# Optimization experiments

Measured on AMD Instinct MI355X. Metric: run time of the kernel, lower is better.

Reference implementation:

```python
import jax, jax.numpy as jnp
import numpy as np

EPS = 1e-7

def sphere_log(p, q):
    # Riemannian log on unit sphere; p, q broadcastable, points along last axis.
    dot = jnp.clip(jnp.sum(p * q, axis=-1, keepdims=True), -1.0 + EPS, 1.0 - EPS)
    theta = jnp.arccos(dot)
    v = q - dot * p                      # tangent direction (unnormalized)
    nv = jnp.linalg.norm(v, axis=-1, keepdims=True)
    nv_safe = jnp.where(nv < EPS, 1.0, nv)
    factor = jnp.where(nv < EPS, 1.0, theta / nv_safe)  # theta/||v|| -> 1 as q->p
    return factor * v

def sphere_exp(p, v):
    # Riemannian exp on unit sphere.
    n = jnp.linalg.norm(v, axis=-1, keepdims=True)
    n_safe = jnp.where(n < EPS, 1.0, n)
    s = jnp.where(n < EPS, 1.0, jnp.sin(n_safe) / n_safe)  # sinc(||v||)
    return jnp.cos(n) * p + s * v

def setup_inputs() -> dict:
    key = jax.random.key(0)
    k1, k2 = jax.random.split(key)
    B, L, C_in, C_out, d = 4, 256, 64, 64, 64
    x = jax.random.normal(k1, (B, L, C_in, d), dtype=jnp.float32)
    x = x / jnp.linalg.norm(x, axis=-1, keepdims=True)  # points on S^{d-1}
    # param 'w': truncated_normal(stddev=1) with shape (n_in, n_out)
    w_raw = jax.random.truncated_normal(k2, -2.0, 2.0, (C_in, C_out), dtype=jnp.float32)
    return {"x": x, "w_raw": w_raw}

def reference(x, w_raw):
    B, L, C_in, d = x.shape
    C_out = w_raw.shape[1]
    # softmax-like positive, column-normalized weights
    w = jnp.exp(w_raw - np.log(C_in).astype(np.float32))
    w = w / w.sum(axis=0)[None]          # (C_in, C_out)

    xr = x.reshape(B * L, C_in, d)       # (N, C_in, d)
    # init at first in-channel point, broadcast over out channels: (N, C_out, d)
    a = jnp.broadcast_to(xr[:, 0][:, None, :], (B * L, C_out, d))

    # 3-step fixed-point iteration toward weighted Frechet mean (scan unroll=3)
    for _ in range(3):
        logs = sphere_log(a[:, :, None, :], xr[:, None, :, :])  # (N, C_out, C_in, d)
        grad = jnp.einsum('io,noid->nod', w, logs)              # (N, C_out, d)
        a = sphere_exp(a, grad)

    return a.reshape(B, L, C_out, d)
```

## Files before the change

kernel.cpp:

```cpp
#include <hip/hip_runtime.h>

#define EPSF 1e-7f
#define TS2 72
#define OFS 68

typedef __bf16 bf16;
typedef __attribute__((ext_vector_type(8))) __bf16 bf16x8;
typedef __attribute__((ext_vector_type(4))) __bf16 bf16x4;
typedef __attribute__((ext_vector_type(4))) float f32x4;

__device__ __forceinline__ float dpp_sum16(float v) {
  int x;
  x = __builtin_amdgcn_update_dpp(0, __builtin_bit_cast(int, v), 0xB1, 0xf, 0xf, true);
  v += __builtin_bit_cast(float, x);
  x = __builtin_amdgcn_update_dpp(0, __builtin_bit_cast(int, v), 0x4E, 0xf, 0xf, true);
  v += __builtin_bit_cast(float, x);
  x = __builtin_amdgcn_update_dpp(0, __builtin_bit_cast(int, v), 0x141, 0xf, 0xf, true);
  v += __builtin_bit_cast(float, x);
  x = __builtin_amdgcn_update_dpp(0, __builtin_bit_cast(int, v), 0x140, 0xf, 0xf, true);
  v += __builtin_bit_cast(float, x);
  return v;
}

__device__ __forceinline__ float fused_factor(float dot) {
  float ax = fabsf(dot);
  float q2 = __builtin_amdgcn_rsqf(1.0f + ax);
  float r2 = __builtin_amdgcn_rsqf(1.0f - ax);
  float pa = fmaf(fmaf(fmaf(-0.0187292994f, ax, 0.0742610070f), ax,
                       -0.2121144013f), ax, 1.5707288f);
  float sel = (dot < 0.0f) ? fmaf(3.14159265358979f, r2, -pa) : pa;
  return sel * q2;
}

__global__ __launch_bounds__(256, 4) void mfd_fc_mfma(
    const float* __restrict__ x, const float* __restrict__ wraw,
    float* __restrict__ out) {
  __shared__ __align__(16) char smem[3 * 64 * TS2 * sizeof(bf16)];
  bf16* Xrow = (bf16*)smem;
  bf16* Xt   = Xrow + 64 * TS2;
  bf16* AC   = Xt + 64 * TS2;
  float* OutF = (float*)smem;

  const int n = blockIdx.x;
  const int tid = threadIdx.x;
  const int wv = tid >> 6;
  const int lane = tid & 63;
  const int ln15 = lane & 15;
  const int quad = lane >> 4;
  const int obase = 16 * wv + 4 * quad;
  const float* xn = x + (size_t)n * 4096;

#pragma unroll
  for (int t = 0; t < 4; ++t) {
    int idx = tid + t * 256;
    int i = idx >> 4;
    int c4 = (idx & 15) << 2;
    float4 v = reinterpret_cast<const float4*>(xn)[idx];
    bf16x4 b;
    b[0] = (bf16)v.x; b[1] = (bf16)v.y; b[2] = (bf16)v.z; b[3] = (bf16)v.w;
    *reinterpret_cast<bf16x4*>(&Xrow[i * TS2 + c4]) = b;
  }

  float wf[4][4];
  {
    float cs[4] = {0.f, 0.f, 0.f, 0.f};
#pragma unroll
    for (int t = 0; t < 4; ++t) {
      float4 wr = *reinterpret_cast<const float4*>(&wraw[(16 * t + ln15) * 64 + obase]);
      wf[t][0] = __expf(wr.x); wf[t][1] = __expf(wr.y);
      wf[t][2] = __expf(wr.z); wf[t][3] = __expf(wr.w);
#pragma unroll
      for (int r = 0; r < 4; ++r) cs[r] += wf[t][r];
    }
#pragma unroll
    for (int r = 0; r < 4; ++r) {
      float inv = __builtin_amdgcn_rcpf(dpp_sum16(cs[r]));
#pragma unroll
      for (int t = 0; t < 4; ++t) wf[t][r] *= inv;
    }
  }

  float a_reg[4][4];
#pragma unroll
  for (int t = 0; t < 4; ++t) {
    float v = xn[16 * t + ln15];
#pragma unroll
    for (int r = 0; r < 4; ++r) a_reg[t][r] = v;
  }
#pragma unroll
  for (int t = 0; t < 4; ++t)
#pragma unroll
    for (int r = 0; r < 4; ++r)
      AC[(obase + r) * TS2 + 16 * t + ln15] = (bf16)a_reg[t][r];

  __syncthreads();

  {
    int dd = tid & 63, ih = tid >> 6;
    bf16 tmp[16];
#pragma unroll
    for (int j = 0; j < 16; ++j) tmp[j] = Xrow[(16 * ih + j) * TS2 + dd];
    *reinterpret_cast<bf16x8*>(&Xt[dd * TS2 + 16 * ih]) =
        *reinterpret_cast<bf16x8*>(&tmp[0]);
    *reinterpret_cast<bf16x8*>(&Xt[dd * TS2 + 16 * ih + 8]) =
        *reinterpret_cast<bf16x8*>(&tmp[8]);
  }

  bf16x8 xrf[4][2];
#pragma unroll
  for (int t = 0; t < 4; ++t)
#pragma unroll
    for (int ks = 0; ks < 2; ++ks)
      xrf[t][ks] = *reinterpret_cast<const bf16x8*>(
          &Xrow[(16 * t + ln15) * TS2 + ks * 32 + quad * 8]);

  const bf16* acbase = &AC[(16 * wv + ln15) * TS2];

  for (int it = 0; it < 3; ++it) {
    f32x4 acc[4] = {f32x4{0,0,0,0}, f32x4{0,0,0,0}, f32x4{0,0,0,0}, f32x4{0,0,0,0}};
#pragma unroll
    for (int ks = 0; ks < 2; ++ks) {
      bf16x8 af = *reinterpret_cast<const bf16x8*>(&acbase[ks * 32 + quad * 8]);
#pragma unroll
      for (int t = 0; t < 4; ++t)
        acc[t] = __builtin_amdgcn_mfma_f32_16x16x32_bf16(af, xrf[t][ks], acc[t], 0, 0, 0);
    }

    float sd[4] = {0.f, 0.f, 0.f, 0.f};
#pragma unroll
    for (int t = 0; t < 4; ++t) {
#pragma unroll
      for (int r = 0; r < 4; ++r) {
        float raw = acc[t][r];
        float dot = __builtin_amdgcn_fmed3f(raw, -1.0f + EPSF, 1.0f - EPSF);
        bf16 cb = (bf16)(wf[t][r] * fused_factor(dot));
        AC[(obase + r) * TS2 + 16 * t + ln15] = cb;
        sd[r] = fmaf((float)cb, dot, sd[r]);
      }
    }
#pragma unroll
    for (int r = 0; r < 4; ++r) sd[r] = dpp_sum16(sd[r]);

    if (it == 0) __syncthreads();

    f32x4 g[4] = {f32x4{0,0,0,0}, f32x4{0,0,0,0}, f32x4{0,0,0,0}, f32x4{0,0,0,0}};
#pragma unroll
    for (int ks = 0; ks < 2; ++ks) {
      bf16x8 af = *reinterpret_cast<const bf16x8*>(&acbase[ks * 32 + quad * 8]);
#pragma unroll
      for (int t = 0; t < 4; ++t) {
        bf16x8 bfr = *reinterpret_cast<const bf16x8*>(
            &Xt[(16 * t + ln15) * TS2 + ks * 32 + quad * 8]);
        g[t] = __builtin_amdgcn_mfma_f32_16x16x32_bf16(af, bfr, g[t], 0, 0, 0);
      }
    }

    float gn2[4] = {0.f, 0.f, 0.f, 0.f};
#pragma unroll
    for (int t = 0; t < 4; ++t)
#pragma unroll
      for (int r = 0; r < 4; ++r) {
        float v = g[t][r] - sd[r] * a_reg[t][r];
        g[t][r] = v;
        gn2[r] = fmaf(v, v, gn2[r]);
      }
#pragma unroll
    for (int r = 0; r < 4; ++r) {
      float nrm = __builtin_amdgcn_sqrtf(dpp_sum16(gn2[r]));
      float rev = nrm * 0.15915494309189535f;
      float sn_ = __builtin_amdgcn_sinf(rev);
      float cn  = __builtin_amdgcn_cosf(rev);
      float sn = (nrm < EPSF) ? 1.0f : sn_ * __builtin_amdgcn_rcpf(nrm);
#pragma unroll
      for (int t = 0; t < 4; ++t)
        a_reg[t][r] = fmaf(cn, a_reg[t][r], sn * g[t][r]);
    }
    if (it < 2) {
#pragma unroll
      for (int t = 0; t < 4; ++t)
#pragma unroll
        for (int r = 0; r < 4; ++r)
          AC[(obase + r) * TS2 + 16 * t + ln15] = (bf16)a_reg[t][r];
    }
  }

  __syncthreads();
#pragma unroll
  for (int t = 0; t < 4; ++t)
#pragma unroll
    for (int r = 0; r < 4; ++r)
      OutF[(obase + r) * OFS + 16 * t + ln15] = a_reg[t][r];
  __syncthreads();
  float* outn = out + (size_t)n * 4096;
#pragma unroll
  for (int t = 0; t < 4; ++t) {
    int idx = tid + t * 256;
    int row = idx >> 4, col4 = (idx & 15) << 2;
    float4 v = *reinterpret_cast<const float4*>(&OutF[row * OFS + col4]);
    reinterpret_cast<float4*>(outn)[idx] = v;
  }
}

extern "C" void kernel_launch(void* const* d_in, const int* in_sizes, int n_in,
                              void* d_out, int out_size, void* d_ws, size_t ws_size,
                              hipStream_t stream) {
  const float* x = (const float*)d_in[0];
  const float* wraw = (const float*)d_in[1];
  float* out = (float*)d_out;
  (void)d_ws; (void)ws_size;

  int N = in_sizes[0] / 4096;
  mfd_fc_mfma<<<N, 256, 0, stream>>>(x, wraw, out);
}
```

Measured before the change: 82.78 us.

## Skip first-iteration MFMA using shared init point and write output directly

At the first iteration every output channel starts from the same point x[0], so the dot products depend only on the input channel. The change computes them with a per-lane bf16 dot and shuffles instead of MFMA plus an AC staging write, and evaluates the arccos factor once per input channel. It also drops the LDS staging of the final output and its two barriers, writing results straight to global memory with 64-byte segments per row rather than float4-coalesced stores. The exchange is less efficient global store patterns for fewer barriers and LDS traffic.

After: 80.59 us. -2.6%, faster.

```diff
diff --git a/kernel.cpp b/kernel.cpp
--- a/kernel.cpp
+++ b/kernel.cpp
@@ -2,7 +2,6 @@
 
 #define EPSF 1e-7f
 #define TS2 72
-#define OFS 68
 
 typedef __bf16 bf16;
 typedef __attribute__((ext_vector_type(8))) __bf16 bf16x8;
@@ -39,7 +38,6 @@
   bf16* Xrow = (bf16*)smem;
   bf16* Xt   = Xrow + 64 * TS2;
   bf16* AC   = Xt + 64 * TS2;
-  float* OutF = (float*)smem;
 
   const int n = blockIdx.x;
   const int tid = threadIdx.x;
@@ -87,13 +85,21 @@
 #pragma unroll
     for (int r = 0; r < 4; ++r) a_reg[t][r] = v;
   }
+
+  __syncthreads();
+
+  bf16x8 xrf[4][2];
 #pragma unroll
   for (int t = 0; t < 4; ++t)
 #pragma unroll
-    for (int r = 0; r < 4; ++r)
-      AC[(obase + r) * TS2 + 16 * t + ln15] = (bf16)a_reg[t][r];
-
-  __syncthreads();
+    for (int ks = 0; ks < 2; ++ks)
+      xrf[t][ks] = *reinterpret_cast<const bf16x8*>(
+          &Xrow[(16 * t + ln15) * TS2 + ks * 32 + quad * 8]);
+
+  bf16x8 x0f[2];
+#pragma unroll
+  for (int ks = 0; ks < 2; ++ks)
+    x0f[ks] = *reinterpret_cast<const bf16x8*>(&Xrow[ks * 32 + quad * 8]);
 
   {
     int dd = tid & 63, ih = tid >> 6;
@@ -106,36 +112,49 @@
         *reinterpret_cast<bf16x8*>(&tmp[8]);
   }
 
-  bf16x8 xrf[4][2];
-#pragma unroll
-  for (int t = 0; t < 4; ++t)
-#pragma unroll
-    for (int ks = 0; ks < 2; ++ks)
-      xrf[t][ks] = *reinterpret_cast<const bf16x8*>(
-          &Xrow[(16 * t + ln15) * TS2 + ks * 32 + quad * 8]);
-
   const bf16* acbase = &AC[(16 * wv + ln15) * TS2];
 
   for (int it = 0; it < 3; ++it) {
-    f32x4 acc[4] = {f32x4{0,0,0,0}, f32x4{0,0,0,0}, f32x4{0,0,0,0}, f32x4{0,0,0,0}};
-#pragma unroll
-    for (int ks = 0; ks < 2; ++ks) {
-      bf16x8 af = *reinterpret_cast<const bf16x8*>(&acbase[ks * 32 + quad * 8]);
-#pragma unroll
-      for (int t = 0; t < 4; ++t)
-        acc[t] = __builtin_amdgcn_mfma_f32_16x16x32_bf16(af, xrf[t][ks], acc[t], 0, 0, 0);
-    }
-
     float sd[4] = {0.f, 0.f, 0.f, 0.f};
-#pragma unroll
-    for (int t = 0; t < 4; ++t) {
-#pragma unroll
-      for (int r = 0; r < 4; ++r) {
-        float raw = acc[t][r];
-        float dot = __builtin_amdgcn_fmed3f(raw, -1.0f + EPSF, 1.0f - EPSF);
-        bf16 cb = (bf16)(wf[t][r] * fused_factor(dot));
-        AC[(obase + r) * TS2 + 16 * t + ln15] = cb;
-        sd[r] = fmaf((float)cb, dot, sd[r]);
+    if (it == 0) {
+#pragma unroll
+      for (int t = 0; t < 4; ++t) {
+        float p = 0.f;
+#pragma unroll
+        for (int ks = 0; ks < 2; ++ks)
+#pragma unroll
+          for (int j = 0; j < 8; ++j)
+            p = fmaf((float)xrf[t][ks][j], (float)x0f[ks][j], p);
+        p += __shfl_xor(p, 16, 64);
+        p += __shfl_xor(p, 32, 64);
+        float d0 = __builtin_amdgcn_fmed3f(p, -1.0f + EPSF, 1.0f - EPSF);
+        float f0 = fused_factor(d0);
+#pragma unroll
+        for (int r = 0; r < 4; ++r) {
+          bf16 cb = (bf16)(wf[t][r] * f0);
+          AC[(obase + r) * TS2 + 16 * t + ln15] = cb;
+          sd[r] = fmaf((float)cb, d0, sd[r]);
+        }
+      }
+    } else {
+      f32x4 acc[4] = {f32x4{0,0,0,0}, f32x4{0,0,0,0}, f32x4{0,0,0,0}, f32x4{0,0,0,0}};
+#pragma unroll
+      for (int ks = 0; ks < 2; ++ks) {
+        bf16x8 af = *reinterpret_cast<const bf16x8*>(&acbase[ks * 32 + quad * 8]);
+#pragma unroll
+        for (int t = 0; t < 4; ++t)
+          acc[t] = __builtin_amdgcn_mfma_f32_16x16x32_bf16(af, xrf[t][ks], acc[t], 0, 0, 0);
+      }
+#pragma unroll
+      for (int t = 0; t < 4; ++t) {
+#pragma unroll
+        for (int r = 0; r < 4; ++r) {
+          float raw = acc[t][r];
+          float dot = __builtin_amdgcn_fmed3f(raw, -1.0f + EPSF, 1.0f - EPSF);
+          bf16 cb = (bf16)(wf[t][r] * fused_factor(dot));
+          AC[(obase + r) * TS2 + 16 * t + ln15] = cb;
+          sd[r] = fmaf((float)cb, dot, sd[r]);
+        }
       }
     }
 #pragma unroll
@@ -174,31 +193,20 @@
 #pragma unroll
       for (int t = 0; t < 4; ++t)
         a_reg[t][r] = fmaf(cn, a_reg[t][r], sn * g[t][r]);
-    }
-    if (it < 2) {
-#pragma unroll
-      for (int t = 0; t < 4; ++t)
-#pragma unroll
-        for (int r = 0; r < 4; ++r)
+      if (it < 2) {
+#pragma unroll
+        for (int t = 0; t < 4; ++t)
           AC[(obase + r) * TS2 + 16 * t + ln15] = (bf16)a_reg[t][r];
-    }
-  }
-
-  __syncthreads();
+      }
+    }
+  }
+
+  float* outn = out + (size_t)n * 4096;
 #pragma unroll
   for (int t = 0; t < 4; ++t)
 #pragma unroll
     for (int r = 0; r < 4; ++r)
-      OutF[(obase + r) * OFS + 16 * t + ln15] = a_reg[t][r];
-  __syncthreads();
-  float* outn = out + (size_t)n * 4096;
-#pragma unroll
-  for (int t = 0; t < 4; ++t) {
-    int idx = tid + t * 256;
-    int row = idx >> 4, col4 = (idx & 15) << 2;
-    float4 v = *reinterpret_cast<const float4*>(&OutF[row * OFS + col4]);
-    reinterpret_cast<float4*>(outn)[idx] = v;
-  }
+      outn[(obase + r) * 64 + 16 * t + ln15] = a_reg[t][r];
 }
 
 extern "C" void kernel_launch(void* const* d_in, const int* in_sizes, int n_in,
```
